# Performance work log

Measured on AMD Instinct MI355X. Metric: run time of the kernel, lower is better.

## Reference

```python
import jax, jax.numpy as jnp
import numpy as np

B, T, C = 2, 2048, 1024
NH = 16
HS = C // NH

def setup_inputs() -> dict:
    key = jax.random.key(0)
    ks = jax.random.split(key, 5)
    x = jax.random.normal(ks[0], (B, T, C), dtype=jnp.float32)
    scale = 1.0 / np.sqrt(C)
    Wk = jax.random.normal(ks[1], (C, C), dtype=jnp.float32) * scale
    bk = jax.random.normal(ks[2], (C,), dtype=jnp.float32) * scale
    Wv = jax.random.normal(ks[3], (C, C), dtype=jnp.float32) * scale
    bv = jax.random.normal(ks[4], (C,), dtype=jnp.float32) * scale
    return {"x": x, "Wk": Wk, "bk": bk, "Wv": Wv, "bv": bv}

def reference(x, Wk, bk, Wv, bv):
    b, t, c = x.shape
    # projections: key and value are Dense; query is identity (as in source)
    k = (x @ Wk + bk).reshape(b, t, NH, HS).transpose(0, 2, 1, 3)  # b nh T hs
    q = x.reshape(b, t, NH, HS).transpose(0, 2, 1, 3)              # b nh T hs
    v = (x @ Wv + bv).reshape(b, t, NH, HS).transpose(0, 2, 1, 3)  # b nh T hs
    # NOTE: source computes logits = K @ Q^T (no 1/sqrt(d) scaling)
    logits = jnp.einsum('bhid,bhjd->bhij', k, q)                   # b nh T T
    causal = jnp.tril(jnp.ones((t, t), dtype=bool))                # True where allowed
    masked = jnp.where(causal[None, None, :, :], logits, -jnp.inf)
    att = jax.nn.softmax(masked, axis=-1)
    y = jnp.einsum('bhij,bhjd->bhid', att, v)                      # b nh T hs
    return y.transpose(0, 2, 1, 3).reshape(b, t, c)
```

## Files before the change

kernel.cpp:

```cpp
#include <hip/hip_runtime.h>
#include <cstdint>
#include <cstddef>

#define BB  2
#define TT  2048
#define CC  1024
#define NHH 16
#define HSS 64
#define BT  (BB*TT)

typedef unsigned short u16;
typedef unsigned int u32;
typedef _Float16 f16;
typedef __attribute__((ext_vector_type(8))) _Float16 f16x8;
typedef __attribute__((ext_vector_type(8))) __bf16 bf16x8;
typedef __attribute__((ext_vector_type(4))) float f32x4;

__device__ __forceinline__ u16 f2bf(float f) {
    union { float f; u32 u; } x; x.f = f;
    return (u16)((x.u + 0x7fffu + ((x.u >> 16) & 1u)) >> 16);
}
__device__ __forceinline__ u16 f2h(float f) {
    union { f16 h; u16 u; } x; x.h = (f16)f;
    return x.u;
}
__device__ __forceinline__ u32 cvtpk_bf16(float lo, float hi) {
    u32 r;
    asm("v_cvt_pk_bf16_f32 %0, %1, %2" : "=v"(r) : "v"(lo), "v"(hi));
    return r;
}

#define MFMA_BF(a,b,c) __builtin_amdgcn_mfma_f32_16x16x32_bf16((a),(b),(c),0,0,0)
#define MFMA_F16(a,b,c) __builtin_amdgcn_mfma_f32_16x16x32_f16((a),(b),(c),0,0,0)

__device__ __forceinline__ void gld16(const u16* g, u16* l) {
    __builtin_amdgcn_global_load_lds(
        (const __attribute__((address_space(1))) unsigned int*)g,
        (__attribute__((address_space(3))) unsigned int*)l, 16, 0, 0);
}

__global__ __launch_bounds__(256) void convert_x(
    const float* __restrict__ X, u16* __restrict__ Xf)
{
    const int idx = (blockIdx.x * 256 + threadIdx.x) * 8;
    const float4 a = *(const float4*)&X[idx];
    const float4 b = *(const float4*)&X[idx + 4];
    float v[8] = {a.x, a.y, a.z, a.w, b.x, b.y, b.z, b.w};
    union { uint4 u; u16 s[8]; } H;
    #pragma unroll
    for (int u = 0; u < 8; ++u) H.s[u] = f2h(v[u]);
    *(uint4*)&Xf[idx] = H.u;
}

__global__ __launch_bounds__(256) void convert_w(
    const float* __restrict__ Wk, const float* __restrict__ Wv,
    u16* __restrict__ WkT, u16* __restrict__ WvT)
{
    const bool isK = (blockIdx.z == 0);
    const float* W = isK ? Wk : Wv;
    u16* WT = isK ? WkT : WvT;
    __shared__ __align__(16) u16 LH[64][72];
    const int tid = threadIdx.x;
    const int k0 = blockIdx.y * 64, n0 = blockIdx.x * 64;
    {
        const int row = tid >> 2, coff = (tid & 3) * 16;
        const float* g = &W[(size_t)(k0 + row) * CC + n0 + coff];
        #pragma unroll
        for (int u = 0; u < 16; ++u) LH[row][coff + u] = f2h(g[u]);
    }
    __syncthreads();
    {
        const int n = tid >> 2, kc = (tid & 3) * 16;
        union { uint4 u[2]; u16 s[16]; } Hq;
        #pragma unroll
        for (int u = 0; u < 16; ++u) Hq.s[u] = LH[kc + u][n];
        uint4* ph = (uint4*)&WT[(size_t)(n0 + n) * CC + k0 + kc];
        ph[0] = Hq.u[0]; ph[1] = Hq.u[1];
    }
}

__global__ __launch_bounds__(256) void proj_kernel(
    const u16* __restrict__ Xf, const u16* __restrict__ WkT,
    const u16* __restrict__ WvT,
    const float* __restrict__ bk, const float* __restrict__ bv,
    u16* __restrict__ Kf, u16* __restrict__ Vt)
{
    __shared__ u16 SM[4][8192];

    const int id = blockIdx.x;
    const int xcd = id & 7, idx = id >> 3;
    const int z = idx >> 5, rem = idx & 31;
    const int n0 = (rem & 7) * 128;
    const int m0 = (xcd * 4 + (rem >> 3)) * 128;
    const bool isK = (z == 0);
    const u16* WT = isK ? WkT : WvT;

    const int tid = threadIdx.x;
    const int w = tid >> 6, lane = tid & 63;
    const int quad = lane >> 4, l15 = lane & 15;
    const int wm = (w >> 1) * 64, wn = (w & 1) * 64;

    const u16* src = (w < 2) ? Xf : WT;
    const int rb = (w < 2) ? m0 : n0;
    int srow[8], scg[8];
    #pragma unroll
    for (int t = 0; t < 8; ++t) {
        int ci = (w & 1) * 512 + t * 64 + lane;
        srow[t] = ci >> 3;
        scg[t] = ((ci & 7) - srow[t]) & 7;
    }
    const int sbase = (w & 1) * 4096;

    f32x4 acc[4][4] = {};

    {
        u16* dst = ((w < 2) ? SM[0] : SM[2]) + sbase;
        #pragma unroll
        for (int t = 0; t < 8; ++t)
            gld16(src + (size_t)(rb + srow[t]) * CC + scg[t] * 8, dst + t * 512);
    }

    for (int ki = 0; ki < 16; ++ki) {
        const int buf = ki & 1;
        __syncthreads();
        if (ki < 15) {
            u16* dst = ((w < 2) ? SM[buf ^ 1] : SM[2 + (buf ^ 1)]) + sbase;
            const int k0n = (ki + 1) * 64;
            #pragma unroll
            for (int t = 0; t < 8; ++t)
                gld16(src + (size_t)(rb + srow[t]) * CC + k0n + scg[t] * 8,
                      dst + t * 512);
        }
        const u16* Ab = SM[buf];
        const u16* Bb = SM[2 + buf];
        #pragma unroll
        for (int kk = 0; kk < 2; ++kk) {
            f16x8 ah[4];
            #pragma unroll
            for (int i = 0; i < 4; ++i) {
                const int row = wm + i * 16 + l15;
                const int cp = ((kk * 4 + quad + row) & 7) * 8;
                ah[i] = *(const f16x8*)&Ab[row * 64 + cp];
            }
            #pragma unroll
            for (int j = 0; j < 4; ++j) {
                const int rowb = wn + j * 16 + l15;
                const int cpb = ((kk * 4 + quad + rowb) & 7) * 8;
                f16x8 bh_ = *(const f16x8*)&Bb[rowb * 64 + cpb];
                #pragma unroll
                for (int i = 0; i < 4; ++i)
                    acc[i][j] = MFMA_F16(ah[i], bh_, acc[i][j]);
            }
        }
    }

    __syncthreads();
    u16* XL = &SM[0][0];

    if (isK) {
        #pragma unroll
        for (int j = 0; j < 4; ++j) {
            const float bias = bk[n0 + wn + j * 16 + l15];
            #pragma unroll
            for (int i = 0; i < 4; ++i)
                #pragma unroll
                for (int r = 0; r < 4; ++r)
                    XL[(wm + i * 16 + quad * 4 + r) * 136 + wn + j * 16 + l15] =
                        f2h(acc[i][j][r] + bias);
        }
        __syncthreads();
        const int r = tid >> 1, half = tid & 1;
        #pragma unroll
        for (int t = 0; t < 8; ++t)
            *(uint4*)&Kf[(size_t)(m0 + r) * CC + n0 + half * 64 + t * 8] =
                *(const uint4*)&XL[r * 136 + half * 64 + t * 8];
    } else {
        #pragma unroll
        for (int j = 0; j < 4; ++j) {
            const float bias = bv[n0 + wn + j * 16 + l15];
            #pragma unroll
            for (int i = 0; i < 4; ++i) {
                uint2 pk;
                pk.x = (u32)f2bf(acc[i][j][0] + bias) |
                       ((u32)f2bf(acc[i][j][1] + bias) << 16);
                pk.y = (u32)f2bf(acc[i][j][2] + bias) |
                       ((u32)f2bf(acc[i][j][3] + bias) << 16);
                *(uint2*)&XL[(wn + j * 16 + l15) * 136 + wm + i * 16 + quad * 4] = pk;
            }
        }
        __syncthreads();
        const int nl = tid >> 1, half = tid & 1;
        const int d = (n0 + nl) & (HSS - 1), hh = (n0 + nl) >> 6;
        const int bb = m0 >> 11, tb = (m0 & (TT - 1)) + half * 64;
        const size_t gb = ((size_t)(bb * NHH + hh) * HSS + d) * TT + tb;
        #pragma unroll
        for (int t = 0; t < 8; ++t)
            *(uint4*)&Vt[gb + t * 8] = *(const uint4*)&XL[nl * 136 + half * 64 + t * 8];
    }
}

__global__ __launch_bounds__(256) void attn_kernel(
    const u16* __restrict__ Xf, const u16* __restrict__ Kf,
    const u16* __restrict__ Vt, float* __restrict__ out)
{
    __shared__ u16 Xs[2][4096];
    __shared__ u16 Vs[2][4096];
    __shared__ __align__(16) u16 Ps[4][2][1152];

    const int L = blockIdx.x;
    const int xcd = L & 7, k = (L >> 3) & 15, grp = L >> 7;
    const int hb = xcd + 8 * grp;
    const int h = hb & (NHH - 1), b = hb >> 4;
    const int iA = k, iB = 31 - k;
    const int i0A = iA * 64, i0B = iB * 64;

    const int tid = threadIdx.x;
    const int w = tid >> 6, lane = tid & 63;
    const int quad = lane >> 4, l15 = lane & 15;
    const size_t rowbase = (size_t)b * TT;
    const int hd = h * HSS;
    const size_t vgbase = (size_t)(b * NHH + h) * HSS * TT;

    bf16x8 ones;
    { union { u32 u[4]; bf16x8 v; } o;
      #pragma unroll
      for (int i = 0; i < 4; ++i) o.u[i] = 0x3F803F80u;
      ones = o.v; }

    f16x8 qA[2], qB[2];
    #pragma unroll
    for (int c = 0; c < 2; ++c) {
        qA[c] = *(const f16x8*)&Kf[(rowbase + i0A + w * 16 + l15) * CC + hd + c * 32 + quad * 8];
        qB[c] = *(const f16x8*)&Kf[(rowbase + i0B + w * 16 + l15) * CC + hd + c * 32 + quad * 8];
    }

    int crow[2], ccg[2], cbase[2];
    #pragma unroll
    for (int t = 0; t < 2; ++t) {
        const int ci = t * 256 + tid;
        crow[t] = ci >> 3;
        ccg[t] = ((ci & 7) - crow[t]) & 7;
        cbase[t] = (t * 256 + w * 64) * 8;
    }
    const u16* gx[2]; const u16* gv[2];
    #pragma unroll
    for (int t = 0; t < 2; ++t) {
        gx[t] = Xf + (rowbase + crow[t]) * CC + hd + ccg[t] * 8;
        gv[t] = Vt + vgbase + (size_t)crow[t] * TT + ccg[t] * 8;
    }

    #pragma unroll
    for (int t = 0; t < 2; ++t) {
        gld16(gx[t], Xs[0] + cbase[t]);
        gld16(gv[t], Vs[0] + cbase[t]);
    }

    f32x4 oA[4] = {}, oB[4] = {};
    f32x4 laA = {}, laB = {};

    for (int jt = 0; jt <= iB; ++jt) {
        const int buf = jt & 1;
        __syncthreads();
        if (jt < iB) {
            const int j0n = (jt + 1) * 64;
            #pragma unroll
            for (int t = 0; t < 2; ++t) {
                gld16(gx[t] + (size_t)j0n * CC, Xs[buf ^ 1] + cbase[t]);
                gld16(gv[t] + j0n, Vs[buf ^ 1] + cbase[t]);
            }
        }
        const bool doA = (jt <= iA);

        f32x4 sB[4], sA[4];
        #pragma unroll
        for (int nt = 0; nt < 4; ++nt) {
            const int krow = nt * 16 + l15;
            f16x8 x0 = *(const f16x8*)&Xs[buf][krow * 64 + ((quad + krow) & 7) * 8];
            f16x8 x1 = *(const f16x8*)&Xs[buf][krow * 64 + ((quad + 4 + krow) & 7) * 8];
            f32x4 z = {-20.f, -20.f, -20.f, -20.f};
            z = MFMA_F16(x0, qB[0], z);
            z = MFMA_F16(x1, qB[1], z);
            sB[nt] = z;
            if (doA) {
                f32x4 y = {-20.f, -20.f, -20.f, -20.f};
                y = MFMA_F16(x0, qA[0], y);
                y = MFMA_F16(x1, qA[1], y);
                sA[nt] = y;
            }
        }
        if (jt == iB) {
            #pragma unroll
            for (int nt = 0; nt < 4; ++nt)
                #pragma unroll
                for (int r = 0; r < 4; ++r)
                    if (nt * 16 + quad * 4 + r > w * 16 + l15) sB[nt][r] = -1e30f;
        }
        if (doA && jt == iA) {
            #pragma unroll
            for (int nt = 0; nt < 4; ++nt)
                #pragma unroll
                for (int r = 0; r < 4; ++r)
                    if (nt * 16 + quad * 4 + r > w * 16 + l15) sA[nt][r] = -1e30f;
        }

        #pragma unroll
        for (int nt = 0; nt < 4; ++nt) {
            const float p0 = __expf(sB[nt][0]);
            const float p1 = __expf(sB[nt][1]);
            const float p2 = __expf(sB[nt][2]);
            const float p3 = __expf(sB[nt][3]);
            uint2 pk;
            pk.x = cvtpk_bf16(p0, p1);
            pk.y = cvtpk_bf16(p2, p3);
            *(uint2*)&Ps[w][0][l15 * 72 + nt * 16 + quad * 4] = pk;
        }
        if (doA) {
            #pragma unroll
            for (int nt = 0; nt < 4; ++nt) {
                const float p0 = __expf(sA[nt][0]);
                const float p1 = __expf(sA[nt][1]);
                const float p2 = __expf(sA[nt][2]);
                const float p3 = __expf(sA[nt][3]);
                uint2 pk;
                pk.x = cvtpk_bf16(p0, p1);
                pk.y = cvtpk_bf16(p2, p3);
                *(uint2*)&Ps[w][1][l15 * 72 + nt * 16 + quad * 4] = pk;
            }
        }

        bf16x8 aB0 = *(const bf16x8*)&Ps[w][0][l15 * 72 + quad * 8];
        bf16x8 aB1 = *(const bf16x8*)&Ps[w][0][l15 * 72 + 32 + quad * 8];
        laB = MFMA_BF(aB0, ones, laB);
        laB = MFMA_BF(aB1, ones, laB);
        bf16x8 aA0, aA1;
        if (doA) {
            aA0 = *(const bf16x8*)&Ps[w][1][l15 * 72 + quad * 8];
            aA1 = *(const bf16x8*)&Ps[w][1][l15 * 72 + 32 + quad * 8];
            laA = MFMA_BF(aA0, ones, laA);
            laA = MFMA_BF(aA1, ones, laA);
        }

        #pragma unroll
        for (int dt = 0; dt < 4; ++dt) {
            const int vrow = dt * 16 + l15;
            bf16x8 v0 = *(const bf16x8*)&Vs[buf][vrow * 64 + ((quad + vrow) & 7) * 8];
            bf16x8 v1 = *(const bf16x8*)&Vs[buf][vrow * 64 + ((quad + 4 + vrow) & 7) * 8];
            oB[dt] = MFMA_BF(aB0, v0, oB[dt]);
            oB[dt] = MFMA_BF(aB1, v1, oB[dt]);
            if (doA) {
                oA[dt] = MFMA_BF(aA0, v0, oA[dt]);
                oA[dt] = MFMA_BF(aA1, v1, oA[dt]);
            }
        }
    }

    float liA[4], liB[4];
    #pragma unroll
    for (int r = 0; r < 4; ++r) { liA[r] = 1.f / laA[r]; liB[r] = 1.f / laB[r]; }
    #pragma unroll
    for (int dt = 0; dt < 4; ++dt) {
        #pragma unroll
        for (int r = 0; r < 4; ++r) {
            const int igA = i0A + w * 16 + quad * 4 + r;
            const int igB = i0B + w * 16 + quad * 4 + r;
            out[(rowbase + igA) * CC + hd + dt * 16 + l15] = oA[dt][r] * liA[r];
            out[(rowbase + igB) * CC + hd + dt * 16 + l15] = oB[dt][r] * liB[r];
        }
    }
}

extern "C" void kernel_launch(void* const* d_in, const int* in_sizes, int n_in,
                              void* d_out, int out_size, void* d_ws, size_t ws_size,
                              hipStream_t stream) {
    (void)in_sizes; (void)n_in; (void)out_size; (void)ws_size;
    const float* x  = (const float*)d_in[0];
    const float* Wk = (const float*)d_in[1];
    const float* bk = (const float*)d_in[2];
    const float* Wv = (const float*)d_in[3];
    const float* bv = (const float*)d_in[4];
    float* out = (float*)d_out;

    const size_t M4 = (size_t)BT * CC;
    const size_t M1 = (size_t)CC * CC;
    u16* Xf  = (u16*)d_ws;
    u16* Kf  = Xf + M4;
    u16* Vt  = Kf + M4;
    u16* WkT = Vt + M4;
    u16* WvT = WkT + M1;

    convert_x<<<dim3(M4 / (256 * 8)), 256, 0, stream>>>(x, Xf);
    convert_w<<<dim3(16, 16, 2), 256, 0, stream>>>(Wk, Wv, WkT, WvT);
    proj_kernel<<<dim3(512), 256, 0, stream>>>(Xf, WkT, WvT, bk, bv, Kf, Vt);
    attn_kernel<<<dim3(512), 256, 0, stream>>>(Xf, Kf, Vt, out);
}
```

Measured before the change: 150.1 us.

## Fuse conversions, deepen projection pipeline, use exp2 and register permlane for P

Merges the x and weight conversion kernels into one launch. Restructures the projection GEMM into a 4-buffer, 32-step pipeline with K=32 slices, explicit vmcnt waits and a new swizzle, and remaps blocks to XCDs. In attention, folds log2(e) into K so exp2 can replace expf, and builds the P operand in registers with permlane16_swap instead of going through LDS, permuting the V read order to match. This removes LDS round trips and launch overhead, at the cost of more complex, fragile waitcnt logic.

```diff
diff --git a/kernel.cpp b/kernel.cpp
--- a/kernel.cpp
+++ b/kernel.cpp
@@ -9,8 +9,12 @@
 #define HSS 64
 #define BT  (BB*TT)
 
+#define LOG2E 1.44269504088896f
+#define S0INIT (-28.8539008f)
+
 typedef unsigned short u16;
 typedef unsigned int u32;
+typedef __attribute__((ext_vector_type(2))) unsigned int u32x2;
 typedef _Float16 f16;
 typedef __attribute__((ext_vector_type(8))) _Float16 f16x8;
 typedef __attribute__((ext_vector_type(8))) __bf16 bf16x8;
@@ -39,29 +43,31 @@
         (__attribute__((address_space(3))) unsigned int*)l, 16, 0, 0);
 }
 
-__global__ __launch_bounds__(256) void convert_x(
-    const float* __restrict__ X, u16* __restrict__ Xf)
-{
-    const int idx = (blockIdx.x * 256 + threadIdx.x) * 8;
-    const float4 a = *(const float4*)&X[idx];
-    const float4 b = *(const float4*)&X[idx + 4];
-    float v[8] = {a.x, a.y, a.z, a.w, b.x, b.y, b.z, b.w};
-    union { uint4 u; u16 s[8]; } H;
-    #pragma unroll
-    for (int u = 0; u < 8; ++u) H.s[u] = f2h(v[u]);
-    *(uint4*)&Xf[idx] = H.u;
-}
-
-__global__ __launch_bounds__(256) void convert_w(
-    const float* __restrict__ Wk, const float* __restrict__ Wv,
+__global__ __launch_bounds__(256) void convert_xw(
+    const float* __restrict__ X, const float* __restrict__ Wk,
+    const float* __restrict__ Wv, u16* __restrict__ Xf,
     u16* __restrict__ WkT, u16* __restrict__ WvT)
 {
-    const bool isK = (blockIdx.z == 0);
+    __shared__ __align__(16) u16 LH[64][72];
+    const int bid = blockIdx.x;
+    const int tid = threadIdx.x;
+    if (bid < 2048) {
+        const int idx = (bid * 256 + tid) * 8;
+        const float4 a = *(const float4*)&X[idx];
+        const float4 b = *(const float4*)&X[idx + 4];
+        float v[8] = {a.x, a.y, a.z, a.w, b.x, b.y, b.z, b.w};
+        union { uint4 u; u16 s[8]; } H;
+        #pragma unroll
+        for (int u = 0; u < 8; ++u) H.s[u] = f2h(v[u]);
+        *(uint4*)&Xf[idx] = H.u;
+        return;
+    }
+    const int bid2 = bid - 2048;
+    const bool isK = (bid2 >> 8) == 0;
+    const int rem = bid2 & 255;
+    const int n0 = (rem & 15) * 64, k0 = (rem >> 4) * 64;
     const float* W = isK ? Wk : Wv;
     u16* WT = isK ? WkT : WvT;
-    __shared__ __align__(16) u16 LH[64][72];
-    const int tid = threadIdx.x;
-    const int k0 = blockIdx.y * 64, n0 = blockIdx.x * 64;
     {
         const int row = tid >> 2, coff = (tid & 3) * 16;
         const float* g = &W[(size_t)(k0 + row) * CC + n0 + coff];
@@ -85,13 +91,14 @@
     const float* __restrict__ bk, const float* __restrict__ bv,
     u16* __restrict__ Kf, u16* __restrict__ Vt)
 {
-    __shared__ u16 SM[4][8192];
+    __shared__ __align__(16) u16 SM[4][8192];
 
     const int id = blockIdx.x;
-    const int xcd = id & 7, idx = id >> 3;
-    const int z = idx >> 5, rem = idx & 31;
-    const int n0 = (rem & 7) * 128;
-    const int m0 = (xcd * 4 + (rem >> 3)) * 128;
+    const int xcd = id & 7;
+    const int z = xcd >> 2, xcd4 = xcd & 3;
+    const int idx = id >> 3;
+    const int n0 = (idx & 7) * 128;
+    const int m0 = (xcd4 * 8 + (idx >> 3)) * 128;
     const bool isK = (z == 0);
     const u16* WT = isK ? WkT : WvT;
 
@@ -101,58 +108,67 @@
     const int wm = (w >> 1) * 64, wn = (w & 1) * 64;
 
     const u16* src = (w < 2) ? Xf : WT;
-    const int rb = (w < 2) ? m0 : n0;
-    int srow[8], scg[8];
-    #pragma unroll
-    for (int t = 0; t < 8; ++t) {
-        int ci = (w & 1) * 512 + t * 64 + lane;
-        srow[t] = ci >> 3;
-        scg[t] = ((ci & 7) - srow[t]) & 7;
-    }
-    const int sbase = (w & 1) * 4096;
+    const int rbase = (w < 2) ? m0 : n0;
+    int srow[4], scg[4];
+    #pragma unroll
+    for (int t = 0; t < 4; ++t) {
+        const int ci = (w & 1) * 256 + t * 64 + lane;
+        const int r = ci >> 2;
+        srow[t] = r;
+        scg[t] = ((ci & 3) - r - (r >> 2)) & 3;
+    }
+    const int dhalf = ((w >= 2) ? 4096 : 0) + (w & 1) * 2048;
+    const u16* gsrc[4];
+    #pragma unroll
+    for (int t = 0; t < 4; ++t)
+        gsrc[t] = src + (size_t)(rbase + srow[t]) * CC + scg[t] * 8;
+
+    const char* smb = (const char*)&SM[0][0];
+    int aoff[4], boff[4];
+    #pragma unroll
+    for (int i = 0; i < 4; ++i) {
+        const int r = wm + i * 16 + l15;
+        aoff[i] = r * 64 + ((quad + r + (r >> 2)) & 3) * 16;
+    }
+    #pragma unroll
+    for (int j = 0; j < 4; ++j) {
+        const int r = wn + j * 16 + l15;
+        boff[j] = 8192 + r * 64 + ((quad + r + (r >> 2)) & 3) * 16;
+    }
 
     f32x4 acc[4][4] = {};
 
-    {
-        u16* dst = ((w < 2) ? SM[0] : SM[2]) + sbase;
-        #pragma unroll
-        for (int t = 0; t < 8; ++t)
-            gld16(src + (size_t)(rb + srow[t]) * CC + scg[t] * 8, dst + t * 512);
-    }
-
-    for (int ki = 0; ki < 16; ++ki) {
-        const int buf = ki & 1;
-        __syncthreads();
-        if (ki < 15) {
-            u16* dst = ((w < 2) ? SM[buf ^ 1] : SM[2 + (buf ^ 1)]) + sbase;
-            const int k0n = (ki + 1) * 64;
-            #pragma unroll
-            for (int t = 0; t < 8; ++t)
-                gld16(src + (size_t)(rb + srow[t]) * CC + k0n + scg[t] * 8,
-                      dst + t * 512);
-        }
-        const u16* Ab = SM[buf];
-        const u16* Bb = SM[2 + buf];
-        #pragma unroll
-        for (int kk = 0; kk < 2; ++kk) {
-            f16x8 ah[4];
-            #pragma unroll
-            for (int i = 0; i < 4; ++i) {
-                const int row = wm + i * 16 + l15;
-                const int cp = ((kk * 4 + quad + row) & 7) * 8;
-                ah[i] = *(const f16x8*)&Ab[row * 64 + cp];
-            }
-            #pragma unroll
-            for (int j = 0; j < 4; ++j) {
-                const int rowb = wn + j * 16 + l15;
-                const int cpb = ((kk * 4 + quad + rowb) & 7) * 8;
-                f16x8 bh_ = *(const f16x8*)&Bb[rowb * 64 + cpb];
-                #pragma unroll
-                for (int i = 0; i < 4; ++i)
-                    acc[i][j] = MFMA_F16(ah[i], bh_, acc[i][j]);
-            }
-        }
-    }
+#define PSTAGE(K, BI)                                                   \
+    { u16* dst = &SM[BI][dhalf];                                        \
+      _Pragma("unroll")                                                 \
+      for (int t = 0; t < 4; ++t)                                       \
+          gld16(gsrc[t] + (K) * 32, dst + t * 512); }
+
+    PSTAGE(0, 0);
+    PSTAGE(1, 1);
+
+    for (int ki = 0; ki < 32; ++ki) {
+        const int buf = ki & 3;
+        if (ki < 30) PSTAGE(ki + 2, (ki + 2) & 3);
+        if (ki < 30)       asm volatile("s_waitcnt vmcnt(8)" ::: "memory");
+        else if (ki == 30) asm volatile("s_waitcnt vmcnt(4)" ::: "memory");
+        else               asm volatile("s_waitcnt vmcnt(0)" ::: "memory");
+        __builtin_amdgcn_sched_barrier(0);
+        __builtin_amdgcn_s_barrier();
+        __builtin_amdgcn_sched_barrier(0);
+        const char* pb = smb + buf * 16384;
+        f16x8 ah[4];
+        #pragma unroll
+        for (int i = 0; i < 4; ++i) ah[i] = *(const f16x8*)(pb + aoff[i]);
+        #pragma unroll
+        for (int j = 0; j < 4; ++j) {
+            f16x8 bh = *(const f16x8*)(pb + boff[j]);
+            #pragma unroll
+            for (int i = 0; i < 4; ++i)
+                acc[i][j] = MFMA_F16(ah[i], bh, acc[i][j]);
+        }
+    }
+#undef PSTAGE
 
     __syncthreads();
     u16* XL = &SM[0][0];
@@ -166,7 +182,7 @@
                 #pragma unroll
                 for (int r = 0; r < 4; ++r)
                     XL[(wm + i * 16 + quad * 4 + r) * 136 + wn + j * 16 + l15] =
-                        f2h(acc[i][j][r] + bias);
+                        f2h((acc[i][j][r] + bias) * LOG2E);
         }
         __syncthreads();
         const int r = tid >> 1, half = tid & 1;
@@ -203,9 +219,8 @@
     const u16* __restrict__ Xf, const u16* __restrict__ Kf,
     const u16* __restrict__ Vt, float* __restrict__ out)
 {
-    __shared__ u16 Xs[2][4096];
-    __shared__ u16 Vs[2][4096];
-    __shared__ __align__(16) u16 Ps[4][2][1152];
+    __shared__ __align__(16) u16 Xs[2][4096];
+    __shared__ __align__(16) u16 Vs[2][4096];
 
     const int L = blockIdx.x;
     const int xcd = L & 7, k = (L >> 3) & 15, grp = L >> 7;
@@ -217,6 +232,7 @@
     const int tid = threadIdx.x;
     const int w = tid >> 6, lane = tid & 63;
     const int quad = lane >> 4, l15 = lane & 15;
+    const int pq = ((quad & 1) << 1) | (quad >> 1);
     const size_t rowbase = (size_t)b * TT;
     const int hd = h * HSS;
     const size_t vgbase = (size_t)(b * NHH + h) * HSS * TT;
@@ -277,12 +293,12 @@
             const int krow = nt * 16 + l15;
             f16x8 x0 = *(const f16x8*)&Xs[buf][krow * 64 + ((quad + krow) & 7) * 8];
             f16x8 x1 = *(const f16x8*)&Xs[buf][krow * 64 + ((quad + 4 + krow) & 7) * 8];
-            f32x4 z = {-20.f, -20.f, -20.f, -20.f};
+            f32x4 z = {S0INIT, S0INIT, S0INIT, S0INIT};
             z = MFMA_F16(x0, qB[0], z);
             z = MFMA_F16(x1, qB[1], z);
             sB[nt] = z;
             if (doA) {
-                f32x4 y = {-20.f, -20.f, -20.f, -20.f};
+                f32x4 y = {S0INIT, S0INIT, S0INIT, S0INIT};
                 y = MFMA_F16(x0, qA[0], y);
                 y = MFMA_F16(x1, qA[1], y);
                 sA[nt] = y;
@@ -303,39 +319,56 @@
                     if (nt * 16 + quad * 4 + r > w * 16 + l15) sA[nt][r] = -1e30f;
         }
 
+        u32 pB_[4][2];
         #pragma unroll
         for (int nt = 0; nt < 4; ++nt) {
-            const float p0 = __expf(sB[nt][0]);
-            const float p1 = __expf(sB[nt][1]);
-            const float p2 = __expf(sB[nt][2]);
-            const float p3 = __expf(sB[nt][3]);
-            uint2 pk;
-            pk.x = cvtpk_bf16(p0, p1);
-            pk.y = cvtpk_bf16(p2, p3);
-            *(uint2*)&Ps[w][0][l15 * 72 + nt * 16 + quad * 4] = pk;
-        }
+            pB_[nt][0] = cvtpk_bf16(exp2f(sB[nt][0]), exp2f(sB[nt][1]));
+            pB_[nt][1] = cvtpk_bf16(exp2f(sB[nt][2]), exp2f(sB[nt][3]));
+        }
+        #pragma unroll
+        for (int c = 0; c < 2; ++c)
+            #pragma unroll
+            for (int p = 0; p < 2; ++p) {
+                u32x2 sw = __builtin_amdgcn_permlane16_swap(
+                    pB_[2 * c][p], pB_[2 * c + 1][p], false, false);
+                pB_[2 * c][p] = sw[0];
+                pB_[2 * c + 1][p] = sw[1];
+            }
+        union { u32 u[4]; bf16x8 v; } ub0, ub1;
+        ub0.u[0] = pB_[0][0]; ub0.u[1] = pB_[0][1];
+        ub0.u[2] = pB_[1][0]; ub0.u[3] = pB_[1][1];
+        ub1.u[0] = pB_[2][0]; ub1.u[1] = pB_[2][1];
+        ub1.u[2] = pB_[3][0]; ub1.u[3] = pB_[3][1];
+        bf16x8 aB0 = ub0.v, aB1 = ub1.v;
+
+        bf16x8 aA0, aA1;
         if (doA) {
+            u32 pA_[4][2];
             #pragma unroll
             for (int nt = 0; nt < 4; ++nt) {
-                const float p0 = __expf(sA[nt][0]);
-                const float p1 = __expf(sA[nt][1]);
-                const float p2 = __expf(sA[nt][2]);
-                const float p3 = __expf(sA[nt][3]);
-                uint2 pk;
-                pk.x = cvtpk_bf16(p0, p1);
-                pk.y = cvtpk_bf16(p2, p3);
-                *(uint2*)&Ps[w][1][l15 * 72 + nt * 16 + quad * 4] = pk;
-            }
-        }
-
-        bf16x8 aB0 = *(const bf16x8*)&Ps[w][0][l15 * 72 + quad * 8];
-        bf16x8 aB1 = *(const bf16x8*)&Ps[w][0][l15 * 72 + 32 + quad * 8];
+                pA_[nt][0] = cvtpk_bf16(exp2f(sA[nt][0]), exp2f(sA[nt][1]));
+                pA_[nt][1] = cvtpk_bf16(exp2f(sA[nt][2]), exp2f(sA[nt][3]));
+            }
+            #pragma unroll
+            for (int c = 0; c < 2; ++c)
+                #pragma unroll
+                for (int p = 0; p < 2; ++p) {
+                    u32x2 sw = __builtin_amdgcn_permlane16_swap(
+                        pA_[2 * c][p], pA_[2 * c + 1][p], false, false);
+                    pA_[2 * c][p] = sw[0];
+                    pA_[2 * c + 1][p] = sw[1];
+                }
+            union { u32 u[4]; bf16x8 v; } ua0, ua1;
+            ua0.u[0] = pA_[0][0]; ua0.u[1] = pA_[0][1];
+            ua0.u[2] = pA_[1][0]; ua0.u[3] = pA_[1][1];
+            ua1.u[0] = pA_[2][0]; ua1.u[1] = pA_[2][1];
+            ua1.u[2] = pA_[3][0]; ua1.u[3] = pA_[3][1];
+            aA0 = ua0.v; aA1 = ua1.v;
+        }
+
         laB = MFMA_BF(aB0, ones, laB);
         laB = MFMA_BF(aB1, ones, laB);
-        bf16x8 aA0, aA1;
         if (doA) {
-            aA0 = *(const bf16x8*)&Ps[w][1][l15 * 72 + quad * 8];
-            aA1 = *(const bf16x8*)&Ps[w][1][l15 * 72 + 32 + quad * 8];
             laA = MFMA_BF(aA0, ones, laA);
             laA = MFMA_BF(aA1, ones, laA);
         }
@@ -343,8 +376,8 @@
         #pragma unroll
         for (int dt = 0; dt < 4; ++dt) {
             const int vrow = dt * 16 + l15;
-            bf16x8 v0 = *(const bf16x8*)&Vs[buf][vrow * 64 + ((quad + vrow) & 7) * 8];
-            bf16x8 v1 = *(const bf16x8*)&Vs[buf][vrow * 64 + ((quad + 4 + vrow) & 7) * 8];
+            bf16x8 v0 = *(const bf16x8*)&Vs[buf][vrow * 64 + ((pq + vrow) & 7) * 8];
+            bf16x8 v1 = *(const bf16x8*)&Vs[buf][vrow * 64 + ((pq + 4 + vrow) & 7) * 8];
             oB[dt] = MFMA_BF(aB0, v0, oB[dt]);
             oB[dt] = MFMA_BF(aB1, v1, oB[dt]);
             if (doA) {
@@ -388,8 +421,7 @@
     u16* WkT = Vt + M4;
     u16* WvT = WkT + M1;
 
-    convert_x<<<dim3(M4 / (256 * 8)), 256, 0, stream>>>(x, Xf);
-    convert_w<<<dim3(16, 16, 2), 256, 0, stream>>>(Wk, Wv, WkT, WvT);
+    convert_xw<<<dim3(2560), 256, 0, stream>>>(x, Wk, Wv, Xf, WkT, WvT);
     proj_kernel<<<dim3(512), 256, 0, stream>>>(Xf, WkT, WvT, bk, bv, Kf, Vt);
     attn_kernel<<<dim3(512), 256, 0, stream>>>(Xf, Kf, Vt, out);
 }
```

Result: slower. 154.2 us (+2.8%).
